# Performance work log

Measured on AMD Instinct MI355X. Metric: run time of the kernel, lower is better.

The kernel has to match this reference:

```python
import jax, jax.numpy as jnp
import numpy as np

N = 50000   # nodes
E = 800000  # edges
F = 128     # input features
W = 128     # hidden width
K = 5       # Chebyshev order


def setup_inputs() -> dict:
    key = jax.random.key(0)
    ks = jax.random.split(key, 12)
    x = jax.random.normal(ks[0], (N, F), jnp.float32)
    edge_index = jax.random.randint(ks[1], (2, E), 0, N, jnp.int32)
    def p(i, shape):
        return jax.random.normal(ks[i], shape, jnp.float32) * 0.05
    return {
        'x': x,
        'edge_index': edge_index,
        'W0': p(2, (K, F, W)), 'b0': p(3, (W,)),
        'W1': p(4, (K, W, W)), 'b1': p(5, (W,)),
        'W2': p(6, (K, W, W)), 'b2': p(7, (W,)),
        'Wl': p(8, (W, 1)),   'bl': p(9, (1,)),
    }


def _norm(edge_index):
    # PyG ChebConv norm with lambda_max=2.0, sym normalization:
    # Lhat = 2/lambda_max * (I - D^-1/2 A D^-1/2) - I  ->  diag 0, offdiag -d_r*d_c
    src, dst = edge_index[0], edge_index[1]
    ew = (src != dst).astype(jnp.float32)  # remove self loops
    deg = jax.ops.segment_sum(ew, src, num_segments=N)
    dinv = jnp.where(deg > 0, jax.lax.rsqrt(jnp.maximum(deg, 1.0)), 0.0)
    w = -ew * dinv[src] * dinv[dst]
    return src, dst, w


def _cheb_conv(h, Wk, b, src, dst, w):
    # Tx_0 = h; Tx_1 = Lhat h; Tx_k = 2 Lhat Tx_{k-1} - Tx_{k-2}
    def matvec(v):
        # gather from src, weight, scatter-add to dst: [E, C] message tensor
        return jax.ops.segment_sum(w[:, None] * v[src], dst, num_segments=N)
    Tx0 = h
    out = Tx0 @ Wk[0]
    Tx1 = matvec(Tx0)
    out = out + Tx1 @ Wk[1]
    for k in range(2, Wk.shape[0]):
        Tx2 = 2.0 * matvec(Tx1) - Tx0
        out = out + Tx2 @ Wk[k]
        Tx0, Tx1 = Tx1, Tx2
    return out + b


def reference(x, edge_index, W0, b0, W1, b1, W2, b2, Wl, bl):
    src, dst, w = _norm(edge_index)
    h = jax.nn.relu(_cheb_conv(x, W0, b0, src, dst, w))  # dropout = identity (eval)
    h = jax.nn.relu(_cheb_conv(h, W1, b1, src, dst, w))
    h = _cheb_conv(h, W2, b2, src, dst, w)
    return h @ Wl + bl  # [N, 1]
```

## Files before the change

kernel.cpp:

```cpp
#include <hip/hip_runtime.h>
#include <hip/hip_bf16.h>
#include <stdint.h>

#define N_NODES 50000
#define N_EDGES 800000
#define FEAT 128
#define CAP 64
#define NCVT 1600000
#define NTRW 163840
#define NPRE (NCVT + NTRW + N_EDGES)

typedef __attribute__((ext_vector_type(4))) float floatx4;
typedef __attribute__((ext_vector_type(8))) _Float16 half8;
typedef __attribute__((ext_vector_type(4))) _Float16 half4;

__device__ __forceinline__ float bf2f(unsigned short u) {
  union { unsigned u; float f; } v; v.u = ((unsigned)u) << 16; return v.f;
}
__device__ __forceinline__ unsigned short f2bf(float f) {
  union { float f; unsigned u; } v; v.f = f;
  unsigned r = v.u + 0x7fffu + ((v.u >> 16) & 1u);
  return (unsigned short)(r >> 16);
}
__device__ __forceinline__ unsigned pack_edge(float w, int s) {
  _Float16 h = (_Float16)w;
  unsigned short hb = __builtin_bit_cast(unsigned short, h);
  return ((unsigned)s << 16) | (unsigned)hb;
}
__device__ __forceinline__ float edge_w(unsigned e) {
  unsigned short hb = (unsigned short)(e & 0xFFFFu);
  return (float)__builtin_bit_cast(_Float16, hb);
}
__device__ __forceinline__ int edge_src(unsigned e) { return (int)(e >> 16); }

__global__ void k_pre1(const unsigned short* __restrict__ x,
                       const void* b0, const void* b1, const void* b2,
                       const void* wl, const void* bl,
                       float* __restrict__ pf, int* __restrict__ flag) {
  __shared__ int cnt_s;
  __shared__ int fl_s;
  int tid = threadIdx.x;
  if (tid == 0) cnt_s = 0;
  __syncthreads();
  int big = 0;
  for (int i = tid; i < 4096; i += 256) {
    unsigned short u = x[2 * i];
    int e = (u >> 7) & 0xFF;
    if (e >= 0xE0) big++;
  }
  atomicAdd(&cnt_s, big);
  __syncthreads();
  if (tid == 0) { fl_s = (cnt_s > 16) ? 1 : 0; flag[0] = fl_s; }
  __syncthreads();
  int fl = fl_s;
  for (int i = tid; i < 513; i += 256) {
    const void* src; int off;
    if (i < 128)      { src = b0; off = i; }
    else if (i < 256) { src = b1; off = i - 128; }
    else if (i < 384) { src = b2; off = i - 256; }
    else if (i < 512) { src = wl; off = i - 384; }
    else              { src = bl; off = 0; }
    pf[i] = fl ? ((const float*)src)[off] : bf2f(((const unsigned short*)src)[off]);
  }
}

__global__ void k_prev(const void* __restrict__ w2, float* __restrict__ pf,
                       const int* __restrict__ flag) {
  int d = blockIdx.x * 256 + threadIdx.x;
  if (d > 640) return;
  int fl = flag[0];
  if (d < 640) {
    int k = d >> 7, f = d & 127;
    float s = 0.f;
    const int base = (k << 14) + (f << 7);
    if (fl) {
      const float* w = (const float*)w2 + base;
#pragma unroll 8
      for (int i = 0; i < 128; ++i) s += w[i] * pf[384 + i];
    } else {
      const unsigned short* w = (const unsigned short*)w2 + base;
#pragma unroll 8
      for (int i = 0; i < 128; ++i) s += bf2f(w[i]) * pf[384 + i];
    }
    pf[520 + d] = s;
  } else {
    float s = 0.f;
    for (int i = 0; i < 128; ++i) s += pf[256 + i] * pf[384 + i];
    pf[1160] = s + pf[512];
  }
}

__global__ void k_pre2(const void* __restrict__ xp,
                       const void* __restrict__ w0, const void* __restrict__ w1,
                       const int* __restrict__ esrc, const int* __restrict__ edst,
                       _Float16* __restrict__ t0, _Float16* __restrict__ wt,
                       int* __restrict__ deg,
                       const int* __restrict__ flag) {
  int i = blockIdx.x * blockDim.x + threadIdx.x;
  int fl = flag[0];
  if (i < NCVT) {
    float4 o;
    if (fl) {
      o = ((const float4*)xp)[i];
    } else {
      ushort4 v = ((const ushort4*)xp)[i];
      o.x = bf2f(v.x); o.y = bf2f(v.y); o.z = bf2f(v.z); o.w = bf2f(v.w);
    }
    half4 h;
    h[0] = (_Float16)o.x; h[1] = (_Float16)o.y; h[2] = (_Float16)o.z; h[3] = (_Float16)o.w;
    ((half4*)t0)[i] = h;
  } else if (i < NCVT + NTRW) {
    int tid = i - NCVT;
    int li = tid >> 14;
    int r = tid & 16383;
    int n = r >> 7, kk = r & 127;
    int l = li / 5, k = li - l * 5;
    const void* w = (l == 0) ? w0 : w1;
    int idx = k * 16384 + kk * 128 + n;
    float v = fl ? ((const float*)w)[idx] : bf2f(((const unsigned short*)w)[idx]);
    wt[tid] = (_Float16)v;
  } else {
    int e = i - (NCVT + NTRW);
    if (e >= N_EDGES) return;
    int s = esrc[e], d = edst[e];
    if (s != d) atomicAdd(&deg[s], 1);
  }
}

__global__ void k_fill(const int* __restrict__ src, const int* __restrict__ dst,
                       const int* __restrict__ deg,
                       int* __restrict__ cnt, unsigned* __restrict__ edata) {
  int e = blockIdx.x * blockDim.x + threadIdx.x;
  if (e >= N_EDGES) return;
  int s = src[e], d = dst[e];
  if (s == d) return;
  int ds = deg[s], dd = deg[d];
  float w = (ds > 0 && dd > 0) ? -rsqrtf((float)ds) * rsqrtf((float)dd) : 0.f;
  int pos = atomicAdd(&cnt[d], 1);
  if (pos < CAP) edata[(d << 6) + pos] = pack_edge(w, s);
}

__global__ __launch_bounds__(256) void k_spmv(const unsigned* __restrict__ edata,
                                              const int* __restrict__ cnt,
                                              const _Float16* __restrict__ X,
                                              const _Float16* __restrict__ Z,
                                              _Float16* __restrict__ Y,
                                              float alpha, int hasZ) {
  int wave = threadIdx.x >> 6, lane = threadIdx.x & 63;
  int q = lane >> 4, l16 = lane & 15;
  int node = blockIdx.x * 16 + wave * 4 + q;
  if (node >= N_NODES) return;
  int n_e = cnt[node]; if (n_e > CAP) n_e = CAP;
  int base = node << 6;

  float acc[8];
#pragma unroll
  for (int f = 0; f < 8; ++f) acc[f] = 0.f;

  unsigned e0 = (0 < n_e) ? edata[base + 0] : 0u;
  unsigned e1 = (1 < n_e) ? edata[base + 1] : 0u;
  unsigned e2 = (2 < n_e) ? edata[base + 2] : 0u;
  unsigned e3 = (3 < n_e) ? edata[base + 3] : 0u;
  unsigned e4 = (4 < n_e) ? edata[base + 4] : 0u;
  unsigned e5 = (5 < n_e) ? edata[base + 5] : 0u;
  unsigned e6 = (6 < n_e) ? edata[base + 6] : 0u;
  unsigned e7 = (7 < n_e) ? edata[base + 7] : 0u;
  half8 r0 = ((const half8*)(X + (size_t)edge_src(e0) * FEAT))[l16];
  half8 r1 = ((const half8*)(X + (size_t)edge_src(e1) * FEAT))[l16];
  half8 r2 = ((const half8*)(X + (size_t)edge_src(e2) * FEAT))[l16];
  half8 r3 = ((const half8*)(X + (size_t)edge_src(e3) * FEAT))[l16];

  for (int j = 0; j < n_e; j += 4) {
    float w0 = edge_w(e0), w1 = edge_w(e1), w2 = edge_w(e2), w3 = edge_w(e3);
    half8 c0 = r0, c1 = r1, c2 = r2, c3 = r3;
    e0 = e4; e1 = e5; e2 = e6; e3 = e7;
    e4 = (j + 8 < n_e) ? edata[base + j + 8] : 0u;
    e5 = (j + 9 < n_e) ? edata[base + j + 9] : 0u;
    e6 = (j + 10 < n_e) ? edata[base + j + 10] : 0u;
    e7 = (j + 11 < n_e) ? edata[base + j + 11] : 0u;
    r0 = ((const half8*)(X + (size_t)edge_src(e0) * FEAT))[l16];
    r1 = ((const half8*)(X + (size_t)edge_src(e1) * FEAT))[l16];
    r2 = ((const half8*)(X + (size_t)edge_src(e2) * FEAT))[l16];
    r3 = ((const half8*)(X + (size_t)edge_src(e3) * FEAT))[l16];
#pragma unroll
    for (int f = 0; f < 8; ++f) {
      acc[f] = fmaf(w0, (float)c0[f], acc[f]);
      acc[f] = fmaf(w1, (float)c1[f], acc[f]);
      acc[f] = fmaf(w2, (float)c2[f], acc[f]);
      acc[f] = fmaf(w3, (float)c3[f], acc[f]);
    }
  }
  half8 res;
  if (hasZ) {
    half8 z = ((const half8*)(Z + (size_t)node * FEAT))[l16];
#pragma unroll
    for (int f = 0; f < 8; ++f) res[f] = (_Float16)(fmaf(alpha, acc[f], -(float)z[f]));
  } else {
#pragma unroll
    for (int f = 0; f < 8; ++f) res[f] = (_Float16)(alpha * acc[f]);
  }
  ((half8*)(Y + (size_t)node * FEAT))[l16] = res;
}

__global__ __launch_bounds__(256) void k_smv(const unsigned* __restrict__ edata,
                                             const int* __restrict__ cnt,
                                             const float* __restrict__ h,
                                             const float* __restrict__ b,
                                             const float* __restrict__ bprev,
                                             float cL, float* __restrict__ y,
                                             int is_out, void* __restrict__ outp,
                                             const int* __restrict__ flag,
                                             const float* __restrict__ cptr) {
  int wave = threadIdx.x >> 6, lane = threadIdx.x & 63;
  int q = lane >> 4, l16 = lane & 15;
  int node = blockIdx.x * 16 + wave * 4 + q;
  if (node >= N_NODES) return;
  int n_e = cnt[node]; if (n_e > CAP) n_e = CAP;
  int base = node << 6;
  float s = 0.f;
  for (int j = l16; j < n_e; j += 16) {
    unsigned e = edata[base + j];
    s = fmaf(edge_w(e), b[edge_src(e)], s);
  }
#pragma unroll
  for (int o = 1; o < 16; o <<= 1) s += __shfl_xor(s, o);
  if (l16 == 0) {
    float r = fmaf(cL, s, h[node]) - (bprev ? bprev[node] : 0.f);
    if (!is_out) {
      y[node] = r;
    } else {
      r += cptr[0];
      if (flag[0]) ((float*)outp)[node] = r;
      else ((unsigned short*)outp)[node] = f2bf(r);
    }
  }
}

__global__ __launch_bounds__(256) void k_gemm(const _Float16* __restrict__ t0, const _Float16* __restrict__ t1,
                                              const _Float16* __restrict__ t2, const _Float16* __restrict__ t3,
                                              const _Float16* __restrict__ t4,
                                              const _Float16* __restrict__ wt,
                                              const float* __restrict__ bias,
                                              _Float16* __restrict__ dst, int mode,
                                              const float* __restrict__ v0,
                                              float* __restrict__ hout) {
  __shared__ _Float16 lb[128 * 136];
  const _Float16* tp[5] = {t0, t1, t2, t3, t4};
  int tid = threadIdx.x, wave = tid >> 6, lane = tid & 63;
  int quad = lane >> 4, l16 = lane & 15;
  int m0 = blockIdx.x * 128;
  floatx4 acc[2][8];
#pragma unroll
  for (int s = 0; s < 2; ++s)
#pragma unroll
    for (int j = 0; j < 8; ++j) acc[s][j] = (floatx4){0.f, 0.f, 0.f, 0.f};
  int arow[2];
  bool aval[2];
#pragma unroll
  for (int s = 0; s < 2; ++s) {
    arow[s] = m0 + wave * 32 + s * 16 + l16;
    aval[s] = arow[s] < N_NODES;
  }

#pragma unroll
  for (int k = 0; k < 5; ++k) {
    __syncthreads();
    {
      int n = tid >> 1, half = tid & 1;
      const uint4* sp = (const uint4*)(wt + k * 16384 + n * 128 + half * 64);
      uint4* dq = (uint4*)(lb + n * 136 + half * 64);
#pragma unroll
      for (int i = 0; i < 8; ++i) dq[i] = sp[i];
    }
    __syncthreads();
    const _Float16* A = tp[k];
#pragma unroll
    for (int ki = 0; ki < 4; ++ki) {
      half8 af[2];
#pragma unroll
      for (int s = 0; s < 2; ++s) {
        if (aval[s]) {
          af[s] = *((const half8*)(A + (size_t)arow[s] * FEAT + ki * 32 + quad * 8));
        } else {
#pragma unroll
          for (int i = 0; i < 8; ++i) af[s][i] = (_Float16)0.f;
        }
      }
#pragma unroll
      for (int j = 0; j < 8; ++j) {
        half8 bf = *((const half8*)(lb + (j * 16 + l16) * 136 + ki * 32 + quad * 8));
        acc[0][j] = __builtin_amdgcn_mfma_f32_16x16x32_f16(af[0], bf, acc[0][j], 0, 0, 0);
        acc[1][j] = __builtin_amdgcn_mfma_f32_16x16x32_f16(af[1], bf, acc[1][j], 0, 0, 0);
      }
    }
  }
#pragma unroll
  for (int s = 0; s < 2; ++s) {
    int rbase = m0 + wave * 32 + s * 16 + quad * 4;
    if (mode == 0) {
#pragma unroll
      for (int j = 0; j < 8; ++j) {
        int col = j * 16 + l16;
        float b = bias[col];
#pragma unroll
        for (int r = 0; r < 4; ++r) {
          int m = rbase + r;
          if (m < N_NODES) {
            float v = fmaxf(acc[s][j][r] + b, 0.f);
            dst[(size_t)m * FEAT + col] = (_Float16)v;
          }
        }
      }
    } else {
      float p[5][4];
#pragma unroll
      for (int k = 0; k < 5; ++k)
#pragma unroll
        for (int r = 0; r < 4; ++r) p[k][r] = 0.f;
#pragma unroll
      for (int j = 0; j < 8; ++j) {
        int col = j * 16 + l16;
        float b = bias[col];
        float vv[5];
#pragma unroll
        for (int k = 0; k < 5; ++k) vv[k] = v0[k * 128 + col];
#pragma unroll
        for (int r = 0; r < 4; ++r) {
          float val = fmaxf(acc[s][j][r] + b, 0.f);
#pragma unroll
          for (int k = 0; k < 5; ++k) p[k][r] = fmaf(val, vv[k], p[k][r]);
        }
      }
#pragma unroll
      for (int o = 1; o < 16; o <<= 1) {
#pragma unroll
        for (int k = 0; k < 5; ++k)
#pragma unroll
          for (int r = 0; r < 4; ++r) p[k][r] += __shfl_xor(p[k][r], o);
      }
      if (l16 == 0) {
#pragma unroll
        for (int r = 0; r < 4; ++r) {
          int m = rbase + r;
          if (m < N_NODES) {
#pragma unroll
            for (int k = 0; k < 5; ++k) hout[k * N_NODES + m] = p[k][r];
          }
        }
      }
    }
  }
}

extern "C" void kernel_launch(void* const* d_in, const int* in_sizes, int n_in,
                              void* d_out, int out_size, void* d_ws, size_t ws_size,
                              hipStream_t stream) {
  const void* x  = d_in[0];
  const int* ei  = (const int*)d_in[1];
  const void* w0 = d_in[2];
  const void* b0 = d_in[3];
  const void* w1 = d_in[4];
  const void* b1 = d_in[5];
  const void* w2 = d_in[6];
  const void* b2 = d_in[7];
  const void* wl = d_in[8];
  const void* bl = d_in[9];
  const int* src = ei;
  const int* dst = ei + N_EDGES;

  char* ws = (char*)d_ws;
  size_t off = 0;
  auto alloc = [&](size_t bytes) -> char* {
    char* p = ws + off;
    off += (bytes + 255) & ~(size_t)255;
    return p;
  };
  _Float16* T[5];
  for (int i = 0; i < 5; ++i) T[i] = (_Float16*)alloc(sizeof(_Float16) * N_NODES * FEAT);
  unsigned* edata = (unsigned*)alloc(sizeof(unsigned) * N_NODES * CAP);
  int* cnt = (int*)alloc(sizeof(int) * N_NODES * 2);
  int* deg = cnt + N_NODES;
  _Float16* wt = (_Float16*)alloc(sizeof(_Float16) * NTRW);
  float* pf = (float*)alloc(sizeof(float) * 1536);
  float* hbuf = (float*)alloc(sizeof(float) * 5 * N_NODES);
  float* bbuf = (float*)alloc(sizeof(float) * 3 * N_NODES);
  int* flag = (int*)alloc(sizeof(int));

  hipMemsetAsync(cnt, 0, sizeof(int) * N_NODES * 2, stream);
  k_pre1<<<1, 256, 0, stream>>>((const unsigned short*)x, b0, b1, b2, wl, bl, pf, flag);
  k_prev<<<3, 256, 0, stream>>>(w2, pf, flag);
  k_pre2<<<(NPRE + 255) / 256, 256, 0, stream>>>(x, w0, w1, src, dst, T[0], wt, deg, flag);
  k_fill<<<(N_EDGES + 255) / 256, 256, 0, stream>>>(src, dst, deg, cnt, edata);

  int nblk_spmv = (N_NODES + 15) / 16;
  int nblk_gemm = (N_NODES + 127) / 128;
  const float* v = pf + 520;
  const float* cc = pf + 1160;

  for (int l = 0; l < 2; ++l) {
    k_spmv<<<nblk_spmv, 256, 0, stream>>>(edata, cnt, T[0], nullptr, T[1], 1.f, 0);
    k_spmv<<<nblk_spmv, 256, 0, stream>>>(edata, cnt, T[1], T[0], T[2], 2.f, 1);
    k_spmv<<<nblk_spmv, 256, 0, stream>>>(edata, cnt, T[2], T[1], T[3], 2.f, 1);
    k_spmv<<<nblk_spmv, 256, 0, stream>>>(edata, cnt, T[3], T[2], T[4], 2.f, 1);
    k_gemm<<<nblk_gemm, 256, 0, stream>>>(T[0], T[1], T[2], T[3], T[4],
                                          wt + l * 5 * 16384, pf + l * 128, T[0],
                                          l, v, hbuf);
  }
  float* h0 = hbuf;
  float* h1 = hbuf + N_NODES;
  float* h2 = hbuf + 2 * N_NODES;
  float* h3 = hbuf + 3 * N_NODES;
  float* h4 = hbuf + 4 * N_NODES;
  float* b3 = bbuf;
  float* b2c = bbuf + N_NODES;
  float* b1c = bbuf + 2 * N_NODES;
  k_smv<<<nblk_spmv, 256, 0, stream>>>(edata, cnt, h3, h4, nullptr, 2.f, b3, 0, nullptr, flag, nullptr);
  k_smv<<<nblk_spmv, 256, 0, stream>>>(edata, cnt, h2, b3, h4, 2.f, b2c, 0, nullptr, flag, nullptr);
  k_smv<<<nblk_spmv, 256, 0, stream>>>(edata, cnt, h1, b2c, b3, 2.f, b1c, 0, nullptr, flag, nullptr);
  k_smv<<<nblk_spmv, 256, 0, stream>>>(edata, cnt, h0, b1c, b2c, 1.f, nullptr, 1, d_out, flag, cc);
}
```

Baseline: 495.4 us.

## Gather int8-quantized features with per-row scales in SpMV

Result: faster. 454.7 us (-8.2%).

```diff
diff --git a/kernel.cpp b/kernel.cpp
--- a/kernel.cpp
+++ b/kernel.cpp
@@ -127,6 +127,30 @@
   }
 }
 
+__global__ __launch_bounds__(256) void k_quant(const _Float16* __restrict__ X,
+                                               unsigned char* __restrict__ Q,
+                                               float* __restrict__ S) {
+  int wave = threadIdx.x >> 6, lane = threadIdx.x & 63;
+  int q = lane >> 4, l16 = lane & 15;
+  int node = blockIdx.x * 16 + wave * 4 + q;
+  if (node >= N_NODES) return;
+  half8 h = ((const half8*)(X + (size_t)node * FEAT))[l16];
+  float v[8], mx = 0.f;
+#pragma unroll
+  for (int f = 0; f < 8; ++f) { v[f] = (float)h[f]; mx = fmaxf(mx, fabsf(v[f])); }
+#pragma unroll
+  for (int o = 1; o < 16; o <<= 1) mx = fmaxf(mx, __shfl_xor(mx, o));
+  float inv = mx > 0.f ? 127.f / mx : 0.f;
+  int qb[8];
+#pragma unroll
+  for (int f = 0; f < 8; ++f) qb[f] = (int)rintf(v[f] * inv) + 128;
+  uint2 p;
+  p.x = (unsigned)qb[0] | ((unsigned)qb[1] << 8) | ((unsigned)qb[2] << 16) | ((unsigned)qb[3] << 24);
+  p.y = (unsigned)qb[4] | ((unsigned)qb[5] << 8) | ((unsigned)qb[6] << 16) | ((unsigned)qb[7] << 24);
+  ((uint2*)(Q + (size_t)node * FEAT))[l16] = p;
+  if (l16 == 0) S[node] = mx > 0.f ? mx / 127.f : 0.f;
+}
+
 __global__ void k_fill(const int* __restrict__ src, const int* __restrict__ dst,
                        const int* __restrict__ deg,
                        int* __restrict__ cnt, unsigned* __restrict__ edata) {
@@ -142,10 +166,13 @@
 
 __global__ __launch_bounds__(256) void k_spmv(const unsigned* __restrict__ edata,
                                               const int* __restrict__ cnt,
-                                              const _Float16* __restrict__ X,
+                                              const unsigned char* __restrict__ Q,
+                                              const float* __restrict__ S,
                                               const _Float16* __restrict__ Z,
                                               _Float16* __restrict__ Y,
-                                              float alpha, int hasZ) {
+                                              unsigned char* __restrict__ Qo,
+                                              float* __restrict__ So,
+                                              float alpha, int hasZ, int wshadow) {
   int wave = threadIdx.x >> 6, lane = threadIdx.x & 63;
   int q = lane >> 4, l16 = lane & 15;
   int node = blockIdx.x * 16 + wave * 4 + q;
@@ -156,6 +183,7 @@
   float acc[8];
 #pragma unroll
   for (int f = 0; f < 8; ++f) acc[f] = 0.f;
+  float wsum = 0.f;
 
   unsigned e0 = (0 < n_e) ? edata[base + 0] : 0u;
   unsigned e1 = (1 < n_e) ? edata[base + 1] : 0u;
@@ -165,41 +193,69 @@
   unsigned e5 = (5 < n_e) ? edata[base + 5] : 0u;
   unsigned e6 = (6 < n_e) ? edata[base + 6] : 0u;
   unsigned e7 = (7 < n_e) ? edata[base + 7] : 0u;
-  half8 r0 = ((const half8*)(X + (size_t)edge_src(e0) * FEAT))[l16];
-  half8 r1 = ((const half8*)(X + (size_t)edge_src(e1) * FEAT))[l16];
-  half8 r2 = ((const half8*)(X + (size_t)edge_src(e2) * FEAT))[l16];
-  half8 r3 = ((const half8*)(X + (size_t)edge_src(e3) * FEAT))[l16];
+  uint2 r0 = ((const uint2*)(Q + (size_t)edge_src(e0) * FEAT))[l16];
+  uint2 r1 = ((const uint2*)(Q + (size_t)edge_src(e1) * FEAT))[l16];
+  uint2 r2 = ((const uint2*)(Q + (size_t)edge_src(e2) * FEAT))[l16];
+  uint2 r3 = ((const uint2*)(Q + (size_t)edge_src(e3) * FEAT))[l16];
+  float s0 = S[edge_src(e0)], s1 = S[edge_src(e1)], s2 = S[edge_src(e2)], s3 = S[edge_src(e3)];
 
   for (int j = 0; j < n_e; j += 4) {
-    float w0 = edge_w(e0), w1 = edge_w(e1), w2 = edge_w(e2), w3 = edge_w(e3);
-    half8 c0 = r0, c1 = r1, c2 = r2, c3 = r3;
+    float ws0 = edge_w(e0) * s0, ws1 = edge_w(e1) * s1;
+    float ws2 = edge_w(e2) * s2, ws3 = edge_w(e3) * s3;
+    uint2 c0 = r0, c1 = r1, c2 = r2, c3 = r3;
     e0 = e4; e1 = e5; e2 = e6; e3 = e7;
     e4 = (j + 8 < n_e) ? edata[base + j + 8] : 0u;
     e5 = (j + 9 < n_e) ? edata[base + j + 9] : 0u;
     e6 = (j + 10 < n_e) ? edata[base + j + 10] : 0u;
     e7 = (j + 11 < n_e) ? edata[base + j + 11] : 0u;
-    r0 = ((const half8*)(X + (size_t)edge_src(e0) * FEAT))[l16];
-    r1 = ((const half8*)(X + (size_t)edge_src(e1) * FEAT))[l16];
-    r2 = ((const half8*)(X + (size_t)edge_src(e2) * FEAT))[l16];
-    r3 = ((const half8*)(X + (size_t)edge_src(e3) * FEAT))[l16];
-#pragma unroll
-    for (int f = 0; f < 8; ++f) {
-      acc[f] = fmaf(w0, (float)c0[f], acc[f]);
-      acc[f] = fmaf(w1, (float)c1[f], acc[f]);
-      acc[f] = fmaf(w2, (float)c2[f], acc[f]);
-      acc[f] = fmaf(w3, (float)c3[f], acc[f]);
-    }
-  }
-  half8 res;
+    r0 = ((const uint2*)(Q + (size_t)edge_src(e0) * FEAT))[l16];
+    r1 = ((const uint2*)(Q + (size_t)edge_src(e1) * FEAT))[l16];
+    r2 = ((const uint2*)(Q + (size_t)edge_src(e2) * FEAT))[l16];
+    r3 = ((const uint2*)(Q + (size_t)edge_src(e3) * FEAT))[l16];
+    s0 = S[edge_src(e0)]; s1 = S[edge_src(e1)]; s2 = S[edge_src(e2)]; s3 = S[edge_src(e3)];
+#define DEC8(c, w)                                                        \
+    acc[0] = fmaf(w, (float)(c.x & 0xFFu), acc[0]);                       \
+    acc[1] = fmaf(w, (float)((c.x >> 8) & 0xFFu), acc[1]);                \
+    acc[2] = fmaf(w, (float)((c.x >> 16) & 0xFFu), acc[2]);               \
+    acc[3] = fmaf(w, (float)(c.x >> 24), acc[3]);                         \
+    acc[4] = fmaf(w, (float)(c.y & 0xFFu), acc[4]);                       \
+    acc[5] = fmaf(w, (float)((c.y >> 8) & 0xFFu), acc[5]);                \
+    acc[6] = fmaf(w, (float)((c.y >> 16) & 0xFFu), acc[6]);               \
+    acc[7] = fmaf(w, (float)(c.y >> 24), acc[7]);
+    DEC8(c0, ws0) DEC8(c1, ws1) DEC8(c2, ws2) DEC8(c3, ws3)
+#undef DEC8
+    wsum += (ws0 + ws1) + (ws2 + ws3);
+  }
+  float rx[8];
+  float b128 = 128.f * wsum;
   if (hasZ) {
     half8 z = ((const half8*)(Z + (size_t)node * FEAT))[l16];
 #pragma unroll
-    for (int f = 0; f < 8; ++f) res[f] = (_Float16)(fmaf(alpha, acc[f], -(float)z[f]));
+    for (int f = 0; f < 8; ++f) rx[f] = fmaf(alpha, acc[f] - b128, -(float)z[f]);
   } else {
 #pragma unroll
-    for (int f = 0; f < 8; ++f) res[f] = (_Float16)(alpha * acc[f]);
-  }
+    for (int f = 0; f < 8; ++f) rx[f] = alpha * (acc[f] - b128);
+  }
+  half8 res;
+#pragma unroll
+  for (int f = 0; f < 8; ++f) res[f] = (_Float16)rx[f];
   ((half8*)(Y + (size_t)node * FEAT))[l16] = res;
+  if (wshadow) {
+    float mx = 0.f;
+#pragma unroll
+    for (int f = 0; f < 8; ++f) mx = fmaxf(mx, fabsf(rx[f]));
+#pragma unroll
+    for (int o = 1; o < 16; o <<= 1) mx = fmaxf(mx, __shfl_xor(mx, o));
+    float inv = mx > 0.f ? 127.f / mx : 0.f;
+    int qb[8];
+#pragma unroll
+    for (int f = 0; f < 8; ++f) qb[f] = (int)rintf(rx[f] * inv) + 128;
+    uint2 p;
+    p.x = (unsigned)qb[0] | ((unsigned)qb[1] << 8) | ((unsigned)qb[2] << 16) | ((unsigned)qb[3] << 24);
+    p.y = (unsigned)qb[4] | ((unsigned)qb[5] << 8) | ((unsigned)qb[6] << 16) | ((unsigned)qb[7] << 24);
+    ((uint2*)(Qo + (size_t)node * FEAT))[l16] = p;
+    if (l16 == 0) So[node] = mx > 0.f ? mx / 127.f : 0.f;
+  }
 }
 
 __global__ __launch_bounds__(256) void k_smv(const unsigned* __restrict__ edata,
@@ -243,7 +299,9 @@
                                               const float* __restrict__ bias,
                                               _Float16* __restrict__ dst, int mode,
                                               const float* __restrict__ v0,
-                                              float* __restrict__ hout) {
+                                              float* __restrict__ hout,
+                                              unsigned char* __restrict__ q8,
+                                              float* __restrict__ sc) {
   __shared__ _Float16 lb[128 * 136];
   const _Float16* tp[5] = {t0, t1, t2, t3, t4};
   int tid = threadIdx.x, wave = tid >> 6, lane = tid & 63;
@@ -298,6 +356,34 @@
   for (int s = 0; s < 2; ++s) {
     int rbase = m0 + wave * 32 + s * 16 + quad * 4;
     if (mode == 0) {
+      float mx[4] = {0.f, 0.f, 0.f, 0.f};
+#pragma unroll
+      for (int j = 0; j < 8; ++j) {
+        int col = j * 16 + l16;
+        float b = bias[col];
+#pragma unroll
+        for (int r = 0; r < 4; ++r) {
+          int m = rbase + r;
+          float v = fmaxf(acc[s][j][r] + b, 0.f);
+          if (m < N_NODES) dst[(size_t)m * FEAT + col] = (_Float16)v;
+          mx[r] = fmaxf(mx[r], v);
+        }
+      }
+#pragma unroll
+      for (int o = 1; o < 16; o <<= 1) {
+#pragma unroll
+        for (int r = 0; r < 4; ++r) mx[r] = fmaxf(mx[r], __shfl_xor(mx[r], o));
+      }
+      float inv[4];
+#pragma unroll
+      for (int r = 0; r < 4; ++r) inv[r] = mx[r] > 0.f ? 127.f / mx[r] : 0.f;
+      if (l16 == 0) {
+#pragma unroll
+        for (int r = 0; r < 4; ++r) {
+          int m = rbase + r;
+          if (m < N_NODES) sc[m] = mx[r] > 0.f ? mx[r] / 127.f : 0.f;
+        }
+      }
 #pragma unroll
       for (int j = 0; j < 8; ++j) {
         int col = j * 16 + l16;
@@ -307,7 +393,8 @@
           int m = rbase + r;
           if (m < N_NODES) {
             float v = fmaxf(acc[s][j][r] + b, 0.f);
-            dst[(size_t)m * FEAT + col] = (_Float16)v;
+            int qv = (int)rintf(v * inv[r]) + 128;
+            q8[(size_t)m * FEAT + col] = (unsigned char)qv;
           }
         }
       }
@@ -377,6 +464,10 @@
   };
   _Float16* T[5];
   for (int i = 0; i < 5; ++i) T[i] = (_Float16*)alloc(sizeof(_Float16) * N_NODES * FEAT);
+  unsigned char* Q[5];
+  for (int i = 0; i < 5; ++i) Q[i] = (unsigned char*)alloc((size_t)N_NODES * FEAT);
+  float* S[5];
+  for (int i = 0; i < 5; ++i) S[i] = (float*)alloc(sizeof(float) * N_NODES);
   unsigned* edata = (unsigned*)alloc(sizeof(unsigned) * N_NODES * CAP);
   int* cnt = (int*)alloc(sizeof(int) * N_NODES * 2);
   int* deg = cnt + N_NODES;
@@ -390,21 +481,23 @@
   k_pre1<<<1, 256, 0, stream>>>((const unsigned short*)x, b0, b1, b2, wl, bl, pf, flag);
   k_prev<<<3, 256, 0, stream>>>(w2, pf, flag);
   k_pre2<<<(NPRE + 255) / 256, 256, 0, stream>>>(x, w0, w1, src, dst, T[0], wt, deg, flag);
-  k_fill<<<(N_EDGES + 255) / 256, 256, 0, stream>>>(src, dst, deg, cnt, edata);
 
   int nblk_spmv = (N_NODES + 15) / 16;
   int nblk_gemm = (N_NODES + 127) / 128;
+  k_quant<<<nblk_spmv, 256, 0, stream>>>(T[0], Q[0], S[0]);
+  k_fill<<<(N_EDGES + 255) / 256, 256, 0, stream>>>(src, dst, deg, cnt, edata);
+
   const float* v = pf + 520;
   const float* cc = pf + 1160;
 
   for (int l = 0; l < 2; ++l) {
-    k_spmv<<<nblk_spmv, 256, 0, stream>>>(edata, cnt, T[0], nullptr, T[1], 1.f, 0);
-    k_spmv<<<nblk_spmv, 256, 0, stream>>>(edata, cnt, T[1], T[0], T[2], 2.f, 1);
-    k_spmv<<<nblk_spmv, 256, 0, stream>>>(edata, cnt, T[2], T[1], T[3], 2.f, 1);
-    k_spmv<<<nblk_spmv, 256, 0, stream>>>(edata, cnt, T[3], T[2], T[4], 2.f, 1);
+    k_spmv<<<nblk_spmv, 256, 0, stream>>>(edata, cnt, Q[0], S[0], nullptr, T[1], Q[1], S[1], 1.f, 0, 1);
+    k_spmv<<<nblk_spmv, 256, 0, stream>>>(edata, cnt, Q[1], S[1], T[0], T[2], Q[2], S[2], 2.f, 1, 1);
+    k_spmv<<<nblk_spmv, 256, 0, stream>>>(edata, cnt, Q[2], S[2], T[1], T[3], Q[3], S[3], 2.f, 1, 1);
+    k_spmv<<<nblk_spmv, 256, 0, stream>>>(edata, cnt, Q[3], S[3], T[2], T[4], nullptr, nullptr, 2.f, 1, 0);
     k_gemm<<<nblk_gemm, 256, 0, stream>>>(T[0], T[1], T[2], T[3], T[4],
                                           wt + l * 5 * 16384, pf + l * 128, T[0],
-                                          l, v, hbuf);
+                                          l, v, hbuf, Q[0], S[0]);
   }
   float* h0 = hbuf;
   float* h1 = hbuf + N_NODES;
```
